# Performance work log

Hardware: AMD Instinct MI355X
Metric: run time of the kernel (lower is better)

The kernel has to match this reference:

```python
import jax, jax.numpy as jnp
import numpy as np

K_MASK = -2.3819763e+38
B, T, D = 2, 2048, 2048
N, K, H = 8, 2, 256          # query heads, kv heads, head dim
F = 8192                     # ffn hidden
A = 4                        # num_altup_inputs
P = 4                        # num_modalities
WINDOW = 512
SOFT_CAP = 50.0
Q_SCALE = H ** -0.5
ROPE_BASE = 10000.0


def rms_norm(x, scale=None, eps=1e-6):
    y = x * jax.lax.rsqrt(jnp.mean(jnp.square(x), axis=-1, keepdims=True) + eps)
    if scale is not None:
        y = y * (1.0 + scale)   # scale_plus_one=True
    return y


def apply_rope(x, pos, base=ROPE_BASE, scale_factor=1.0):
    # x: [B,T,num_heads,H], pos: [B,T]
    h = x.shape[-1]
    frac = 2.0 * jnp.arange(h // 2, dtype=jnp.float32) / h
    timescale = base ** frac
    sin_inp = (pos[..., None].astype(jnp.float32) / timescale)[..., None, :] / scale_factor  # [B,T,1,H/2]
    sin, cos = jnp.sin(sin_inp), jnp.cos(sin_inp)
    x1, x2 = jnp.split(x, 2, axis=-1)
    return jnp.concatenate([x1 * cos - x2 * sin, x2 * cos + x1 * sin], axis=-1).astype(x.dtype)


def setup_inputs():
    key = jax.random.key(0)
    ks = jax.random.split(key, 12)
    r = lambda i, shape, s=0.02: jax.random.normal(ks[i], shape, dtype=jnp.float32) * s
    pos = jnp.broadcast_to(jnp.arange(T, dtype=jnp.int32), (B, T))
    causal = pos[:, :, None] >= pos[:, None, :]  # [B,T,T] bool
    return dict(
        x=jax.random.normal(ks[0], (A, B, T, D), dtype=jnp.float32),
        segment_pos=pos,
        attn_mask=causal,
        router_w=r(1, (D, P), 1.0),
        pred_coefs=r(2, (P, A, A), 0.0001),
        corr_coefs=r(3, (P, A), 0.01),
        correct_output_scale=jnp.ones((D,), jnp.float32),
        pre_attn_scale=jnp.zeros((D,), jnp.float32),
        q_w=r(4, (N, D, H)),
        kv_w=r(5, (2, K, D, H)),
        qk_q_scale=jnp.zeros((H,), jnp.float32),
        qk_k_scale=jnp.zeros((H,), jnp.float32),
        o_w=r(6, (N, H, D)),
        post_attn_scale=jnp.zeros((D,), jnp.float32),
        pre_ffw_scale=jnp.zeros((D,), jnp.float32),
        gate_w=r(7, (D, F)),
        up_w=r(8, (D, F)),
        down_w=r(9, (F, D)),
        post_ffw_scale=jnp.zeros((D,), jnp.float32),
    )


def _router(h, router_w):
    # modality router: scale by 1/d_model, project, tanh in fp32
    return jnp.tanh(jnp.einsum('btd,dp->btp', h * (1.0 / D), router_w).astype(jnp.float32))


def _attention(x, segment_pos, attn_mask, q_w, kv_w, qk_q_scale, qk_k_scale, o_w):
    q = jnp.einsum('btd,ndh->btnh', x, q_w)               # [B,T,N,H]
    k, v = jnp.einsum('bsd,ckdh->cbskh', x, kv_w)         # each [B,T,K,H]
    q = rms_norm(q, qk_q_scale)                           # qk norm
    k = rms_norm(k, qk_k_scale)
    v = rms_norm(v)                                       # value norm (no scale)
    q = apply_rope(q, segment_pos) * Q_SCALE
    k = apply_rope(k, segment_pos)
    g = N // K                                            # GQA group size
    qr = q.reshape(B, T, K, g, H)
    logits = jnp.einsum('btkgh,bskh->btkgs', qr, k).reshape(B, T, N, T)
    logits = jnp.tanh(logits / SOFT_CAP) * SOFT_CAP       # attn_logits_soft_cap
    # sliding-window mask combined with causal attn_mask
    sliding = (segment_pos[:, None, :] > segment_pos[:, :, None] - WINDOW) & \
              (segment_pos[:, None, :] < segment_pos[:, :, None] + WINDOW)
    mask = attn_mask & sliding
    padded = jnp.where(mask[:, :, None, :], logits, K_MASK)
    probs = jax.nn.softmax(padded, axis=-1).astype(k.dtype)
    enc = jnp.einsum('btkgs,bskh->btkgh', probs.reshape(B, T, K, g, T), v).reshape(B, T, N, H)
    return jnp.einsum('btnh,nhd->btd', enc, o_w)


def reference(x, segment_pos, attn_mask, router_w, pred_coefs, corr_coefs,
              correct_output_scale, pre_attn_scale, q_w, kv_w, qk_q_scale, qk_k_scale,
              o_w, post_attn_scale, pre_ffw_scale, gate_w, up_w, down_w, post_ffw_scale):
    # ---- AltUp predict ----
    mods = _router(x[0], router_w)                                   # [B,T,P]
    coefs = jnp.einsum('btp,pij->btij', mods, pred_coefs.astype(jnp.float32))
    predictions = x + jnp.einsum('btij,jbtd->ibtd', coefs, x).astype(x.dtype)
    active = predictions[0]
    # ---- attention block ----
    attn_in = rms_norm(active, pre_attn_scale)
    attn = _attention(attn_in, segment_pos, attn_mask, q_w, kv_w, qk_q_scale, qk_k_scale, o_w)
    attn = rms_norm(attn, post_attn_scale)
    attn_gated = active + attn
    # ---- gated-GELU MLP ----
    h = rms_norm(attn_gated, pre_ffw_scale)
    ffw = jnp.einsum('btf,fd->btd', jax.nn.gelu(h @ gate_w) * (h @ up_w), down_w)
    ffw = rms_norm(ffw, post_ffw_scale)
    activated = attn_gated + ffw
    # ---- AltUp correct (with scale_corrected_output) ----
    activated = activated * correct_output_scale
    mods_c = _router(activated, router_w)
    c = jnp.einsum('btp,pi->bti', mods_c, corr_coefs.astype(jnp.float32)) + 1.0
    innovation = activated - predictions[0]
    corrected = predictions + jnp.einsum('bti,btd->ibtd', c, innovation).astype(x.dtype)
    return corrected
```

## Files before the change

### kernel.cpp

```cpp
#include <hip/hip_runtime.h>
#include <hip/hip_bf16.h>

typedef unsigned short u16;
typedef __attribute__((ext_vector_type(8))) short bf16x8_t;
typedef __attribute__((ext_vector_type(4))) float f32x4_t;

#define DEV __device__ __forceinline__

constexpr int cB = 2, cT = 2048, cD = 2048;
constexpr int cN = 8, cK = 2, cH = 256, cF = 8192;
constexpr int cBT = cB * cT;
constexpr float cEPS = 1e-6f;
constexpr float cQS = 0.0625f;
constexpr float cCAP = 50.0f;
constexpr int cWIN = 512;
constexpr int cNH = 12;

DEV u16 f2bf(float f) {
  union { float f; unsigned u; } c; c.f = f;
  unsigned u = c.u;
  return (u16)((u + 0x7fffu + ((u >> 16) & 1u)) >> 16);
}
DEV float bf2f(u16 h) {
  union { unsigned u; float f; } c; c.u = ((unsigned)h) << 16;
  return c.f;
}

DEV float block_sum256(float v, float* sbuf) {
  #pragma unroll
  for (int m = 32; m > 0; m >>= 1) v += __shfl_xor(v, m, 64);
  int wid = threadIdx.x >> 6;
  if ((threadIdx.x & 63) == 0) sbuf[wid] = v;
  __syncthreads();
  float tot = sbuf[0] + sbuf[1] + sbuf[2] + sbuf[3];
  __syncthreads();
  return tot;
}

#define GLD_LDS16(gp, lp) __builtin_amdgcn_global_load_lds( \
    (const __attribute__((address_space(1))) void*)(gp),    \
    (__attribute__((address_space(3))) void*)(lp), 16, 0, 0)

#define WAITV(n) asm volatile("s_waitcnt vmcnt(" #n ")" ::: "memory")
#define LGKM0()  asm volatile("s_waitcnt lgkmcnt(0)" ::: "memory")

__global__ __launch_bounds__(256) void k_transpose_cast(
    const float* __restrict__ src, u16* __restrict__ dst, int R, int C) {
  __shared__ float tile[32][33];
  size_t base = (size_t)blockIdx.z * R * C;
  int c0 = blockIdx.x * 32, r0 = blockIdx.y * 32;
  int tx = threadIdx.x & 31, ty = threadIdx.x >> 5;
  #pragma unroll
  for (int i = 0; i < 4; i++)
    tile[ty + i * 8][tx] = src[base + (size_t)(r0 + ty + i * 8) * C + c0 + tx];
  __syncthreads();
  #pragma unroll
  for (int i = 0; i < 4; i++)
    dst[base + (size_t)(c0 + ty + i * 8) * R + r0 + tx] = f2bf(tile[tx][ty + i * 8]);
}

__global__ __launch_bounds__(256) void k_predict(
    const float* __restrict__ x, const float* __restrict__ router_w,
    const float* __restrict__ pred_coefs, const float* __restrict__ pre_attn_scale,
    float* __restrict__ out, u16* __restrict__ attn_in) {
  __shared__ float sbuf[4];
  int bt = blockIdx.x, tid = threadIdx.x;
  const size_t PL = (size_t)cBT * cD;
  const size_t rowb = (size_t)bt * cD;
  float xv[4][8];
  #pragma unroll
  for (int j = 0; j < 4; j++)
    #pragma unroll
    for (int u = 0; u < 8; u++)
      xv[j][u] = x[j * PL + rowb + u * 256 + tid];
  float rp0 = 0, rp1 = 0, rp2 = 0, rp3 = 0;
  #pragma unroll
  for (int u = 0; u < 8; u++) {
    const float4 rw = *(const float4*)(router_w + (size_t)(u * 256 + tid) * 4);
    rp0 += xv[0][u] * rw.x; rp1 += xv[0][u] * rw.y;
    rp2 += xv[0][u] * rw.z; rp3 += xv[0][u] * rw.w;
  }
  float mods[4];
  mods[0] = tanhf(block_sum256(rp0, sbuf) * (1.0f / cD));
  mods[1] = tanhf(block_sum256(rp1, sbuf) * (1.0f / cD));
  mods[2] = tanhf(block_sum256(rp2, sbuf) * (1.0f / cD));
  mods[3] = tanhf(block_sum256(rp3, sbuf) * (1.0f / cD));
  float coef[4][4];
  #pragma unroll
  for (int i = 0; i < 4; i++)
    #pragma unroll
    for (int j = 0; j < 4; j++) {
      float s = 0;
      #pragma unroll
      for (int p = 0; p < 4; p++) s += mods[p] * pred_coefs[(p * 4 + i) * 4 + j];
      coef[i][j] = s;
    }
  float p0[8], ssq = 0;
  #pragma unroll
  for (int u = 0; u < 8; u++) {
    #pragma unroll
    for (int i = 0; i < 4; i++) {
      float s = xv[i][u];
      #pragma unroll
      for (int j = 0; j < 4; j++) s += coef[i][j] * xv[j][u];
      out[i * PL + rowb + u * 256 + tid] = s;
      if (i == 0) { p0[u] = s; ssq += s * s; }
    }
  }
  float rs = rsqrtf(block_sum256(ssq, sbuf) * (1.0f / cD) + cEPS);
  #pragma unroll
  for (int u = 0; u < 8; u++) {
    int d = u * 256 + tid;
    attn_in[rowb + d] = f2bf(p0[u] * rs * (1.0f + pre_attn_scale[d]));
  }
}

template <int MI, int OUT_BF16>
__global__ __launch_bounds__(512, 2) void k_gemm8(
    const u16* __restrict__ A, const u16* __restrict__ Bt, void* __restrict__ Cv,
    int Nn, int Kk) {
  static_assert(MI == 4 || MI == 8, "");
  constexpr int BM = MI * 32;
  constexpr int A_KS = BM * 32;
  constexpr int B_KS = 256 * 32;
  constexpr int BUF_E = 2 * A_KS + 2 * B_KS;
  extern __shared__ u16 lds[];

  const int tid = threadIdx.x;
  const int wid = tid >> 6, lane = tid & 63;
  const int wr = wid >> 2, wc = wid & 3;
  const int fr = lane & 15, fq = lane >> 4;

  const int nwg = gridDim.x * gridDim.y;
  const int flat = blockIdx.y * gridDim.x + blockIdx.x;
  const int swz = (flat & 7) * (nwg >> 3) + (flat >> 3);
  const int m0 = (swz % gridDim.x) * BM;
  const int n0 = (swz / gridDim.x) * 256;
  const int NT = Kk >> 6;

  const int srow = lane >> 2, sslot = lane & 3;

  auto stageA = [&](int t, int ks) {
    u16* buf = lds + (t & 1) * BUF_E + ks * A_KS;
    #pragma unroll
    for (int i = 0; i < BM / 128; i++) {
      int row0 = i * 128 + wid * 16;
      int row = row0 + srow;
      int col = (sslot ^ ((row >> 1) & 3)) * 8;
      GLD_LDS16(A + (size_t)(m0 + row) * Kk + t * 64 + ks * 32 + col, buf + row0 * 32);
    }
  };
  auto stageB = [&](int t, int ks) {
    u16* buf = lds + (t & 1) * BUF_E + 2 * A_KS + ks * B_KS;
    #pragma unroll
    for (int i = 0; i < 2; i++) {
      int row0 = i * 128 + wid * 16;
      int row = row0 + srow;
      int col = (sslot ^ ((row >> 1) & 3)) * 8;
      GLD_LDS16(Bt + (size_t)(n0 + row) * Kk + t * 64 + ks * 32 + col, buf + row0 * 32);
    }
  };
  auto readA = [&](const u16* buf, int ks, int i) -> bf16x8_t {
    int row = wr * (MI * 16) + i * 16 + fr;
    return *(const bf16x8_t*)(buf + ks * A_KS + row * 32 + (fq ^ ((row >> 1) & 3)) * 8);
  };
  auto readB = [&](const u16* buf, int ks, int j) -> bf16x8_t {
    int row = wc * 64 + j * 16 + fr;
    return *(const bf16x8_t*)(buf + 2 * A_KS + ks * B_KS + row * 32 + (fq ^ ((row >> 1) & 3)) * 8);
  };

  f32x4_t acc[MI][4];
  #pragma unroll
  for (int i = 0; i < MI; i++)
    #pragma unroll
    for (int j = 0; j < 4; j++) acc[i][j] = (f32x4_t){0.f, 0.f, 0.f, 0.f};

  stageA(0, 0); stageB(0, 0); stageA(0, 1); stageB(0, 1);
  if constexpr (MI == 8) WAITV(4); else WAITV(3);
  __builtin_amdgcn_s_barrier();

#define PHASE_MFMA(J0)                                                              \
  __builtin_amdgcn_s_setprio(1);                                                    \
  _Pragma("unroll")                                                                 \
  for (int i = 0; i < MI; i++) {                                                    \
    acc[i][J0]     = __builtin_amdgcn_mfma_f32_16x16x32_bf16(a0[i], b0[0], acc[i][J0], 0, 0, 0);     \
    acc[i][J0 + 1] = __builtin_amdgcn_mfma_f32_16x16x32_bf16(a0[i], b0[1], acc[i][J0 + 1], 0, 0, 0); \
  }                                                                                 \
  __builtin_amdgcn_s_setprio(0);

  for (int t = 0; t < NT; t++) {
    const u16* buf = lds + (t & 1) * BUF_E;
    const bool pf = (t + 1 < NT);
    bf16x8_t a0[MI], b0[2];

    #pragma unroll
    for (int i = 0; i < MI; i++) a0[i] = readA(buf, 0, i);
    b0[0] = readB(buf, 0, 0); b0[1] = readB(buf, 0, 1);
    if (pf) stageA(t + 1, 0);
    __builtin_amdgcn_s_barrier();
    LGKM0(); __builtin_amdgcn_sched_barrier(0);
    PHASE_MFMA(0)
    __builtin_amdgcn_s_barrier();

    b0[0] = readB(buf, 0, 2); b0[1] = readB(buf, 0, 3);
    if (pf) stageB(t + 1, 0);
    if (pf) { if constexpr (MI == 8) WAITV(4); else WAITV(3); } else WAITV(0);
    __builtin_amdgcn_s_barrier();
    LGKM0(); __builtin_amdgcn_sched_barrier(0);
    PHASE_MFMA(2)
    __builtin_amdgcn_s_barrier();

    #pragma unroll
    for (int i = 0; i < MI; i++) a0[i] = readA(buf, 1, i);
    b0[0] = readB(buf, 1, 0); b0[1] = readB(buf, 1, 1);
    if (pf) stageA(t + 1, 1);
    __builtin_amdgcn_s_barrier();
    LGKM0(); __builtin_amdgcn_sched_barrier(0);
    PHASE_MFMA(0)
    __builtin_amdgcn_s_barrier();

    b0[0] = readB(buf, 1, 2); b0[1] = readB(buf, 1, 3);
    if (pf) stageB(t + 1, 1);
    if (pf) { if constexpr (MI == 8) WAITV(4); else WAITV(3); }
    __builtin_amdgcn_s_barrier();
    LGKM0(); __builtin_amdgcn_sched_barrier(0);
    PHASE_MFMA(2)
    __builtin_amdgcn_s_barrier();
  }
#undef PHASE_MFMA

  #pragma unroll
  for (int i = 0; i < MI; i++)
    #pragma unroll
    for (int j = 0; j < 4; j++)
      #pragma unroll
      for (int r = 0; r < 4; r++) {
        int m = m0 + wr * (MI * 16) + i * 16 + fq * 4 + r;
        int n = n0 + wc * 64 + j * 16 + fr;
        float v = acc[i][j][r];
        if (OUT_BF16) ((u16*)Cv)[(size_t)m * Nn + n] = f2bf(v);
        else ((float*)Cv)[(size_t)m * Nn + n] = v;
      }
}

__global__ __launch_bounds__(64) void k_qkpost(
    u16* __restrict__ buf, const float* __restrict__ scale, const int* __restrict__ pos,
    int heads, int tokstride, int headoff, float oscale) {
  int hidx = blockIdx.x % heads, bt = blockIdx.x / heads;
  int lane = threadIdx.x;
  u16* row = buf + ((size_t)bt * tokstride + headoff + hidx) * cH;
  float v[4], ssq = 0;
  #pragma unroll
  for (int m = 0; m < 4; m++) { v[m] = bf2f(row[lane + 64 * m]); ssq += v[m] * v[m]; }
  #pragma unroll
  for (int mm = 32; mm > 0; mm >>= 1) ssq += __shfl_xor(ssq, mm, 64);
  float rs = rsqrtf(ssq * (1.0f / cH) + cEPS);
  #pragma unroll
  for (int m = 0; m < 4; m++) {
    int e = lane + 64 * m;
    v[m] = v[m] * rs * (1.0f + scale[e]);
  }
  float p = (float)pos[bt];
  #pragma unroll
  for (int m = 0; m < 2; m++) {
    int j = lane + 64 * m;
    float ts = powf(10000.0f, (2.0f * j) * (1.0f / cH));
    float si = p / ts;
    float sn = sinf(si), cs = cosf(si);
    float x1 = v[m], x2 = v[m + 2];
    row[j]       = f2bf((x1 * cs - x2 * sn) * oscale);
    row[j + 128] = f2bf((x2 * cs + x1 * sn) * oscale);
  }
}

__global__ __launch_bounds__(64) void k_vpost(
    const u16* __restrict__ qkv, u16* __restrict__ vT) {
  int kk = blockIdx.x % cK, bt = blockIdx.x / cK;
  int b = bt / cT, t = bt % cT;
  int lane = threadIdx.x;
  const u16* row = qkv + ((size_t)bt * cNH + 10 + kk) * cH;
  float v[4], ssq = 0;
  #pragma unroll
  for (int m = 0; m < 4; m++) { v[m] = bf2f(row[lane + 64 * m]); ssq += v[m] * v[m]; }
  #pragma unroll
  for (int mm = 32; mm > 0; mm >>= 1) ssq += __shfl_xor(ssq, mm, 64);
  float rs = rsqrtf(ssq * (1.0f / cH) + cEPS);
  #pragma unroll
  for (int m = 0; m < 4; m++) {
    int e = lane + 64 * m;
    vT[((size_t)(b * cK + kk) * cH + e) * cT + t] = f2bf(v[m] * rs);
  }
}

__global__ __launch_bounds__(64) void k_attn(
    const u16* __restrict__ qkv, const u16* __restrict__ vT, u16* __restrict__ enc) {
  int t0 = blockIdx.x * 16;
  int n = blockIdx.y, b = blockIdx.z;
  int kn = n >> 2;
  int lane = threadIdx.x;
  int fr = lane & 15, fq = lane >> 4;
  __shared__ float P[16][32];

  bf16x8_t qf[8];
  const u16* qrow = qkv + ((size_t)(b * cT + t0 + fr) * cNH + n) * cH;
  #pragma unroll
  for (int ks = 0; ks < 8; ks++) qf[ks] = *(const bf16x8_t*)(qrow + ks * 32 + fq * 8);

  f32x4_t acc[16];
  #pragma unroll
  for (int ht = 0; ht < 16; ht++) acc[ht] = (f32x4_t){0.f, 0.f, 0.f, 0.f};
  float psum[4] = {0.f, 0.f, 0.f, 0.f};

  int s_lo = t0 - (cWIN - 1); if (s_lo < 0) s_lo = 0; s_lo &= ~31;
  for (int s0 = s_lo; s0 <= t0 + 15; s0 += 32) {
    f32x4_t S[2];
    S[0] = (f32x4_t){0.f, 0.f, 0.f, 0.f};
    S[1] = (f32x4_t){0.f, 0.f, 0.f, 0.f};
    #pragma unroll
    for (int c = 0; c < 2; c++) {
      const u16* krow = qkv + ((size_t)(b * cT + s0 + c * 16 + fr) * cNH + 8 + kn) * cH;
      #pragma unroll
      for (int ks = 0; ks < 8; ks++) {
        bf16x8_t kf = *(const bf16x8_t*)(krow + ks * 32 + fq * 8);
        S[c] = __builtin_amdgcn_mfma_f32_16x16x32_bf16(qf[ks], kf, S[c], 0, 0, 0);
      }
    }
    #pragma unroll
    for (int c = 0; c < 2; c++) {
      int s = s0 + c * 16 + fr;
      #pragma unroll
      for (int r = 0; r < 4; r++) {
        int t = t0 + fq * 4 + r;
        float l = S[c][r];
        l = tanhf(l * (1.0f / cCAP)) * cCAP;
        float pe = (s <= t && s >= t - (cWIN - 1)) ? __expf(l) : 0.0f;
        psum[r] += pe;
        P[fq * 4 + r][c * 16 + fr] = pe;
      }
    }
    bf16x8_t pf;
    #pragma unroll
    for (int e = 0; e < 8; e++) pf[e] = (short)f2bf(P[fr][fq * 8 + e]);
    #pragma unroll
    for (int ht = 0; ht < 16; ht++) {
      bf16x8_t vf = *(const bf16x8_t*)(vT + (((size_t)(b * cK + kn)) * cH + ht * 16 + fr) * cT + s0 + fq * 8);
      acc[ht] = __builtin_amdgcn_mfma_f32_16x16x32_bf16(pf, vf, acc[ht], 0, 0, 0);
    }
  }
  #pragma unroll
  for (int r = 0; r < 4; r++) {
    #pragma unroll
    for (int m = 1; m < 16; m <<= 1) psum[r] += __shfl_xor(psum[r], m, 64);
  }
  float inv[4];
  #pragma unroll
  for (int r = 0; r < 4; r++) inv[r] = 1.0f / psum[r];
  #pragma unroll
  for (int ht = 0; ht < 16; ht++)
    #pragma unroll
    for (int r = 0; r < 4; r++)
      enc[(((size_t)(b * cT + t0 + fq * 4 + r)) * cN + n) * cH + ht * 16 + fr] =
          f2bf(acc[ht][r] * inv[r]);
}

__global__ __launch_bounds__(256) void k_postattn(
    const float* __restrict__ attn_raw, const float* __restrict__ out0,
    const float* __restrict__ post_attn_scale, const float* __restrict__ pre_ffw_scale,
    float* __restrict__ ag, u16* __restrict__ h) {
  __shared__ float sbuf[4];
  int bt = blockIdx.x, tid = threadIdx.x;
  const size_t rowb = (size_t)bt * cD;
  float ar[8], ssq = 0;
  #pragma unroll
  for (int u = 0; u < 8; u++) { ar[u] = attn_raw[rowb + u * 256 + tid]; ssq += ar[u] * ar[u]; }
  float rs = rsqrtf(block_sum256(ssq, sbuf) * (1.0f / cD) + cEPS);
  float agv[8], ssq2 = 0;
  #pragma unroll
  for (int u = 0; u < 8; u++) {
    int d = u * 256 + tid;
    float a = out0[rowb + d] + ar[u] * rs * (1.0f + post_attn_scale[d]);
    agv[u] = a;
    ag[rowb + d] = a;
    ssq2 += a * a;
  }
  float rs2 = rsqrtf(block_sum256(ssq2, sbuf) * (1.0f / cD) + cEPS);
  #pragma unroll
  for (int u = 0; u < 8; u++) {
    int d = u * 256 + tid;
    h[rowb + d] = f2bf(agv[u] * rs2 * (1.0f + pre_ffw_scale[d]));
  }
}

__global__ __launch_bounds__(256) void k_gelumul(
    const u16* __restrict__ GU, u16* __restrict__ Ap) {
  size_t i = (size_t)blockIdx.x * 256 + threadIdx.x;
  size_t row = i >> 10, col8 = i & 1023;
  const u16* gp = GU + row * (2 * cF) + col8 * 8;
  bf16x8_t g8 = *(const bf16x8_t*)gp;
  bf16x8_t u8 = *(const bf16x8_t*)(gp + cF);
  bf16x8_t o;
  #pragma unroll
  for (int e = 0; e < 8; e++) {
    float xg = bf2f((u16)g8[e]);
    float xu = bf2f((u16)u8[e]);
    float t = 0.5f * xg * (1.0f + tanhf(0.7978845608f * (xg + 0.044715f * xg * xg * xg)));
    o[e] = (short)f2bf(t * xu);
  }
  *(bf16x8_t*)(Ap + row * cF + col8 * 8) = o;
}

__global__ __launch_bounds__(256) void k_final(
    const float* __restrict__ ffw_raw, const float* __restrict__ ag,
    const float* __restrict__ post_ffw_scale, const float* __restrict__ cos_scale,
    const float* __restrict__ router_w, const float* __restrict__ corr_coefs,
    float* __restrict__ out) {
  __shared__ float sbuf[4];
  int bt = blockIdx.x, tid = threadIdx.x;
  const size_t PL = (size_t)cBT * cD;
  const size_t rowb = (size_t)bt * cD;
  float fv[8], ssq = 0;
  #pragma unroll
  for (int u = 0; u < 8; u++) { fv[u] = ffw_raw[rowb + u * 256 + tid]; ssq += fv[u] * fv[u]; }
  float rs = rsqrtf(block_sum256(ssq, sbuf) * (1.0f / cD) + cEPS);
  float av[8];
  float rp0 = 0, rp1 = 0, rp2 = 0, rp3 = 0;
  #pragma unroll
  for (int u = 0; u < 8; u++) {
    int d = u * 256 + tid;
    float a = (ag[rowb + d] + fv[u] * rs * (1.0f + post_ffw_scale[d])) * cos_scale[d];
    av[u] = a;
    const float4 rw = *(const float4*)(router_w + (size_t)d * 4);
    rp0 += a * rw.x; rp1 += a * rw.y; rp2 += a * rw.z; rp3 += a * rw.w;
  }
  float mods[4];
  mods[0] = tanhf(block_sum256(rp0, sbuf) * (1.0f / cD));
  mods[1] = tanhf(block_sum256(rp1, sbuf) * (1.0f / cD));
  mods[2] = tanhf(block_sum256(rp2, sbuf) * (1.0f / cD));
  mods[3] = tanhf(block_sum256(rp3, sbuf) * (1.0f / cD));
  float cc[4];
  #pragma unroll
  for (int i = 0; i < 4; i++) {
    float s = 1.0f;
    #pragma unroll
    for (int p = 0; p < 4; p++) s += mods[p] * corr_coefs[p * 4 + i];
    cc[i] = s;
  }
  #pragma unroll
  for (int u = 0; u < 8; u++) {
    size_t o = rowb + u * 256 + tid;
    float p0v = out[o];
    float innov = av[u] - p0v;
    out[o] = p0v + cc[0] * innov;
    out[PL + o]     += cc[1] * innov;
    out[2 * PL + o] += cc[2] * innov;
    out[3 * PL + o] += cc[3] * innov;
  }
}

extern "C" void kernel_launch(void* const* d_in, const int* in_sizes, int n_in,
                              void* d_out, int out_size, void* d_ws, size_t ws_size,
                              hipStream_t stream) {
  const float* x              = (const float*)d_in[0];
  const int*   pos            = (const int*)d_in[1];
  const float* router_w       = (const float*)d_in[3];
  const float* pred_coefs     = (const float*)d_in[4];
  const float* corr_coefs     = (const float*)d_in[5];
  const float* cos_scale      = (const float*)d_in[6];
  const float* pre_attn_scale = (const float*)d_in[7];
  const float* q_w            = (const float*)d_in[8];
  const float* kv_w           = (const float*)d_in[9];
  const float* qk_q_scale     = (const float*)d_in[10];
  const float* qk_k_scale     = (const float*)d_in[11];
  const float* o_w            = (const float*)d_in[12];
  const float* post_attn_scale= (const float*)d_in[13];
  const float* pre_ffw_scale  = (const float*)d_in[14];
  const float* gate_w         = (const float*)d_in[15];
  const float* up_w           = (const float*)d_in[16];
  const float* down_w         = (const float*)d_in[17];
  const float* post_ffw_scale = (const float*)d_in[18];
  float* out = (float*)d_out;

  char* wsp = (char*)d_ws;
  size_t off = 0;
  auto take = [&](size_t nbytes) -> char* {
    char* p = wsp + off;
    off += (nbytes + 255) & ~((size_t)255);
    return p;
  };
  u16* gu_wT    = (u16*)take((size_t)2 * cF * cD * 2);
  u16* down_wT  = (u16*)take((size_t)cD * cF * 2);
  u16* qkv_wT   = (u16*)take((size_t)cNH * cH * cD * 2);
  u16* o_wT     = (u16*)take((size_t)cD * cN * cH * 2);
  u16* attn_in  = (u16*)take((size_t)cBT * cD * 2);
  u16* qkvbuf   = (u16*)take((size_t)cBT * cNH * cH * 2);
  u16* vTbuf    = (u16*)take((size_t)cB * cK * cH * cT * 2);
  u16* encbuf   = (u16*)take((size_t)cBT * cN * cH * 2);
  float* attn_raw = (float*)take((size_t)cBT * cD * 4);
  float* agbuf    = (float*)take((size_t)cBT * cD * 4);
  u16* hbuf     = (u16*)take((size_t)cBT * cD * 2);
  u16* GUbuf    = (u16*)take((size_t)cBT * 2 * cF * 2);
  u16* Gcbuf    = (u16*)take((size_t)cBT * cF * 2);
  float* ffw_raw = (float*)take((size_t)cBT * cD * 4);
  (void)in_sizes; (void)n_in; (void)out_size; (void)ws_size;

  dim3 blk256(256), blk64(64), blk512(512);
  constexpr unsigned LDS8 = 2 * (2 * 256 * 32 + 2 * 256 * 32) * 2;
  constexpr unsigned LDS4 = 2 * (2 * 128 * 32 + 2 * 256 * 32) * 2;

  k_transpose_cast<<<dim3(cF / 32, cD / 32, 1), blk256, 0, stream>>>(gate_w, gu_wT, cD, cF);
  k_transpose_cast<<<dim3(cF / 32, cD / 32, 1), blk256, 0, stream>>>(up_w, gu_wT + (size_t)cF * cD, cD, cF);
  k_transpose_cast<<<dim3(cD / 32, cF / 32, 1), blk256, 0, stream>>>(down_w, down_wT, cF, cD);
  k_transpose_cast<<<dim3(cH / 32, cD / 32, cN), blk256, 0, stream>>>(q_w, qkv_wT, cD, cH);
  k_transpose_cast<<<dim3(cH / 32, cD / 32, 2 * cK), blk256, 0, stream>>>(
      kv_w, qkv_wT + (size_t)cN * cH * cD, cD, cH);
  k_transpose_cast<<<dim3(cD / 32, (cN * cH) / 32, 1), blk256, 0, stream>>>(o_w, o_wT, cN * cH, cD);

  k_predict<<<dim3(cBT), blk256, 0, stream>>>(x, router_w, pred_coefs, pre_attn_scale, out, attn_in);

  k_gemm8<4, 1><<<dim3(cBT / 128, (cNH * cH) / 256), blk512, LDS4, stream>>>(
      attn_in, qkv_wT, qkvbuf, cNH * cH, cD);

  k_qkpost<<<dim3(cBT * cN), blk64, 0, stream>>>(qkvbuf, qk_q_scale, pos, cN, cNH, 0, cQS);
  k_qkpost<<<dim3(cBT * cK), blk64, 0, stream>>>(qkvbuf, qk_k_scale, pos, cK, cNH, 8, 1.0f);
  k_vpost<<<dim3(cBT * cK), blk64, 0, stream>>>(qkvbuf, vTbuf);

  k_attn<<<dim3(cT / 16, cN, cB), blk64, 0, stream>>>(qkvbuf, vTbuf, encbuf);

  k_gemm8<4, 0><<<dim3(cBT / 128, cD / 256), blk512, LDS4, stream>>>(
      encbuf, o_wT, attn_raw, cD, cN * cH);
  k_postattn<<<dim3(cBT), blk256, 0, stream>>>(attn_raw, out, post_attn_scale, pre_ffw_scale, agbuf, hbuf);

  k_gemm8<8, 1><<<dim3(cBT / 256, (2 * cF) / 256), blk512, LDS8, stream>>>(
      hbuf, gu_wT, GUbuf, 2 * cF, cD);
  k_gelumul<<<dim3((unsigned)(((size_t)cBT * cF / 8) / 256)), blk256, 0, stream>>>(GUbuf, Gcbuf);
  k_gemm8<4, 0><<<dim3(cBT / 128, cD / 256), blk512, LDS4, stream>>>(
      Gcbuf, down_wT, ffw_raw, cD, cF);

  k_final<<<dim3(cBT), blk256, 0, stream>>>(ffw_raw, agbuf, post_ffw_scale, cos_scale,
                                            router_w, corr_coefs, out);
}
```

Baseline: 1.046 ms.

## Fuse GELU-gate multiply into gate/up GEMM epilogue via interleaved weights; vectorize row kernels

```diff
diff --git a/kernel.cpp b/kernel.cpp
--- a/kernel.cpp
+++ b/kernel.cpp
@@ -25,6 +25,15 @@
   union { unsigned u; float f; } c; c.u = ((unsigned)h) << 16;
   return c.f;
 }
+DEV float g4(const float4& v, int k) { return k == 0 ? v.x : k == 1 ? v.y : k == 2 ? v.z : v.w; }
+DEV void store_bf4(u16* p, float a, float b, float c, float d) {
+  union { u16 h[4]; uint2 v; } o;
+  o.h[0] = f2bf(a); o.h[1] = f2bf(b); o.h[2] = f2bf(c); o.h[3] = f2bf(d);
+  *(uint2*)p = o.v;
+}
+DEV float gelu_tanh(float x) {
+  return 0.5f * x * (1.0f + tanhf(0.7978845608f * (x + 0.044715f * x * x * x)));
+}
 
 DEV float block_sum256(float v, float* sbuf) {
   #pragma unroll
@@ -45,7 +54,7 @@
 #define LGKM0()  asm volatile("s_waitcnt lgkmcnt(0)" ::: "memory")
 
 __global__ __launch_bounds__(256) void k_transpose_cast(
-    const float* __restrict__ src, u16* __restrict__ dst, int R, int C) {
+    const float* __restrict__ src, u16* __restrict__ dst, int R, int C, int gu) {
   __shared__ float tile[32][33];
   size_t base = (size_t)blockIdx.z * R * C;
   int c0 = blockIdx.x * 32, r0 = blockIdx.y * 32;
@@ -55,8 +64,11 @@
     tile[ty + i * 8][tx] = src[base + (size_t)(r0 + ty + i * 8) * C + c0 + tx];
   __syncthreads();
   #pragma unroll
-  for (int i = 0; i < 4; i++)
-    dst[base + (size_t)(c0 + ty + i * 8) * R + r0 + tx] = f2bf(tile[tx][ty + i * 8]);
+  for (int i = 0; i < 4; i++) {
+    int c = c0 + ty + i * 8;
+    int n = (gu < 0) ? c : (((c >> 4) << 5) + (gu << 4) + (c & 15));
+    dst[base + (size_t)n * R + r0 + tx] = f2bf(tile[tx][ty + i * 8]);
+  }
 }
 
 __global__ __launch_bounds__(256) void k_predict(
@@ -67,24 +79,25 @@
   int bt = blockIdx.x, tid = threadIdx.x;
   const size_t PL = (size_t)cBT * cD;
   const size_t rowb = (size_t)bt * cD;
-  float xv[4][8];
+  float4 xv[4][2];
   #pragma unroll
   for (int j = 0; j < 4; j++)
     #pragma unroll
-    for (int u = 0; u < 8; u++)
-      xv[j][u] = x[j * PL + rowb + u * 256 + tid];
-  float rp0 = 0, rp1 = 0, rp2 = 0, rp3 = 0;
-  #pragma unroll
-  for (int u = 0; u < 8; u++) {
-    const float4 rw = *(const float4*)(router_w + (size_t)(u * 256 + tid) * 4);
-    rp0 += xv[0][u] * rw.x; rp1 += xv[0][u] * rw.y;
-    rp2 += xv[0][u] * rw.z; rp3 += xv[0][u] * rw.w;
-  }
+    for (int u = 0; u < 2; u++)
+      xv[j][u] = *(const float4*)(x + j * PL + rowb + (u * 256 + tid) * 4);
+  float rp[4] = {0, 0, 0, 0};
+  #pragma unroll
+  for (int u = 0; u < 2; u++)
+    #pragma unroll
+    for (int k = 0; k < 4; k++) {
+      int e = (u * 256 + tid) * 4 + k;
+      float4 rw = *(const float4*)(router_w + (size_t)e * 4);
+      float xe = g4(xv[0][u], k);
+      rp[0] += xe * rw.x; rp[1] += xe * rw.y; rp[2] += xe * rw.z; rp[3] += xe * rw.w;
+    }
   float mods[4];
-  mods[0] = tanhf(block_sum256(rp0, sbuf) * (1.0f / cD));
-  mods[1] = tanhf(block_sum256(rp1, sbuf) * (1.0f / cD));
-  mods[2] = tanhf(block_sum256(rp2, sbuf) * (1.0f / cD));
-  mods[3] = tanhf(block_sum256(rp3, sbuf) * (1.0f / cD));
+  #pragma unroll
+  for (int p = 0; p < 4; p++) mods[p] = tanhf(block_sum256(rp[p], sbuf) * (1.0f / cD));
   float coef[4][4];
   #pragma unroll
   for (int i = 0; i < 4; i++)
@@ -95,27 +108,32 @@
       for (int p = 0; p < 4; p++) s += mods[p] * pred_coefs[(p * 4 + i) * 4 + j];
       coef[i][j] = s;
     }
-  float p0[8], ssq = 0;
-  #pragma unroll
-  for (int u = 0; u < 8; u++) {
+  float4 p04[2]; float ssq = 0;
+  #pragma unroll
+  for (int u = 0; u < 2; u++)
     #pragma unroll
     for (int i = 0; i < 4; i++) {
-      float s = xv[i][u];
+      float4 s = xv[i][u];
       #pragma unroll
-      for (int j = 0; j < 4; j++) s += coef[i][j] * xv[j][u];
-      out[i * PL + rowb + u * 256 + tid] = s;
-      if (i == 0) { p0[u] = s; ssq += s * s; }
-    }
-  }
+      for (int j = 0; j < 4; j++) {
+        s.x += coef[i][j] * xv[j][u].x; s.y += coef[i][j] * xv[j][u].y;
+        s.z += coef[i][j] * xv[j][u].z; s.w += coef[i][j] * xv[j][u].w;
+      }
+      *(float4*)(out + i * PL + rowb + (u * 256 + tid) * 4) = s;
+      if (i == 0) { p04[u] = s; ssq += s.x * s.x + s.y * s.y + s.z * s.z + s.w * s.w; }
+    }
   float rs = rsqrtf(block_sum256(ssq, sbuf) * (1.0f / cD) + cEPS);
   #pragma unroll
-  for (int u = 0; u < 8; u++) {
-    int d = u * 256 + tid;
-    attn_in[rowb + d] = f2bf(p0[u] * rs * (1.0f + pre_attn_scale[d]));
-  }
-}
-
-template <int MI, int OUT_BF16>
+  for (int u = 0; u < 2; u++) {
+    int e0 = (u * 256 + tid) * 4;
+    float4 sc = *(const float4*)(pre_attn_scale + e0);
+    store_bf4(attn_in + rowb + e0,
+              p04[u].x * rs * (1.0f + sc.x), p04[u].y * rs * (1.0f + sc.y),
+              p04[u].z * rs * (1.0f + sc.z), p04[u].w * rs * (1.0f + sc.w));
+  }
+}
+
+template <int MI, int OUT_MODE>
 __global__ __launch_bounds__(512, 2) void k_gemm8(
     const u16* __restrict__ A, const u16* __restrict__ Bt, void* __restrict__ Cv,
     int Nn, int Kk) {
@@ -229,18 +247,34 @@
   }
 #undef PHASE_MFMA
 
-  #pragma unroll
-  for (int i = 0; i < MI; i++)
-    #pragma unroll
-    for (int j = 0; j < 4; j++)
+  if constexpr (OUT_MODE == 2) {
+    const int Nh = Nn >> 1;
+    #pragma unroll
+    for (int i = 0; i < MI; i++)
       #pragma unroll
-      for (int r = 0; r < 4; r++) {
-        int m = m0 + wr * (MI * 16) + i * 16 + fq * 4 + r;
-        int n = n0 + wc * 64 + j * 16 + fr;
-        float v = acc[i][j][r];
-        if (OUT_BF16) ((u16*)Cv)[(size_t)m * Nn + n] = f2bf(v);
-        else ((float*)Cv)[(size_t)m * Nn + n] = v;
+      for (int jp = 0; jp < 2; jp++) {
+        int c = (n0 + wc * 64 + jp * 32) / 2 + fr;
+        #pragma unroll
+        for (int r = 0; r < 4; r++) {
+          int m = m0 + wr * (MI * 16) + i * 16 + fq * 4 + r;
+          float g = acc[i][2 * jp][r], uu = acc[i][2 * jp + 1][r];
+          ((u16*)Cv)[(size_t)m * Nh + c] = f2bf(gelu_tanh(g) * uu);
+        }
       }
+  } else {
+    #pragma unroll
+    for (int i = 0; i < MI; i++)
+      #pragma unroll
+      for (int j = 0; j < 4; j++)
+        #pragma unroll
+        for (int r = 0; r < 4; r++) {
+          int m = m0 + wr * (MI * 16) + i * 16 + fq * 4 + r;
+          int n = n0 + wc * 64 + j * 16 + fr;
+          float v = acc[i][j][r];
+          if (OUT_MODE == 1) ((u16*)Cv)[(size_t)m * Nn + n] = f2bf(v);
+          else ((float*)Cv)[(size_t)m * Nn + n] = v;
+        }
+  }
 }
 
 __global__ __launch_bounds__(64) void k_qkpost(
@@ -370,43 +404,37 @@
   __shared__ float sbuf[4];
   int bt = blockIdx.x, tid = threadIdx.x;
   const size_t rowb = (size_t)bt * cD;
-  float ar[8], ssq = 0;
-  #pragma unroll
-  for (int u = 0; u < 8; u++) { ar[u] = attn_raw[rowb + u * 256 + tid]; ssq += ar[u] * ar[u]; }
+  float4 ar[2]; float ssq = 0;
+  #pragma unroll
+  for (int u = 0; u < 2; u++) {
+    ar[u] = *(const float4*)(attn_raw + rowb + (u * 256 + tid) * 4);
+    ssq += ar[u].x * ar[u].x + ar[u].y * ar[u].y + ar[u].z * ar[u].z + ar[u].w * ar[u].w;
+  }
   float rs = rsqrtf(block_sum256(ssq, sbuf) * (1.0f / cD) + cEPS);
-  float agv[8], ssq2 = 0;
-  #pragma unroll
-  for (int u = 0; u < 8; u++) {
-    int d = u * 256 + tid;
-    float a = out0[rowb + d] + ar[u] * rs * (1.0f + post_attn_scale[d]);
+  float4 agv[2]; float ssq2 = 0;
+  #pragma unroll
+  for (int u = 0; u < 2; u++) {
+    int e0 = (u * 256 + tid) * 4;
+    float4 o0 = *(const float4*)(out0 + rowb + e0);
+    float4 sc = *(const float4*)(post_attn_scale + e0);
+    float4 a;
+    a.x = o0.x + ar[u].x * rs * (1.0f + sc.x);
+    a.y = o0.y + ar[u].y * rs * (1.0f + sc.y);
+    a.z = o0.z + ar[u].z * rs * (1.0f + sc.z);
+    a.w = o0.w + ar[u].w * rs * (1.0f + sc.w);
     agv[u] = a;
-    ag[rowb + d] = a;
-    ssq2 += a * a;
+    *(float4*)(ag + rowb + e0) = a;
+    ssq2 += a.x * a.x + a.y * a.y + a.z * a.z + a.w * a.w;
   }
   float rs2 = rsqrtf(block_sum256(ssq2, sbuf) * (1.0f / cD) + cEPS);
   #pragma unroll
-  for (int u = 0; u < 8; u++) {
-    int d = u * 256 + tid;
-    h[rowb + d] = f2bf(agv[u] * rs2 * (1.0f + pre_ffw_scale[d]));
-  }
-}
-
-__global__ __launch_bounds__(256) void k_gelumul(
-    const u16* __restrict__ GU, u16* __restrict__ Ap) {
-  size_t i = (size_t)blockIdx.x * 256 + threadIdx.x;
-  size_t row = i >> 10, col8 = i & 1023;
-  const u16* gp = GU + row * (2 * cF) + col8 * 8;
-  bf16x8_t g8 = *(const bf16x8_t*)gp;
-  bf16x8_t u8 = *(const bf16x8_t*)(gp + cF);
-  bf16x8_t o;
-  #pragma unroll
-  for (int e = 0; e < 8; e++) {
-    float xg = bf2f((u16)g8[e]);
-    float xu = bf2f((u16)u8[e]);
-    float t = 0.5f * xg * (1.0f + tanhf(0.7978845608f * (xg + 0.044715f * xg * xg * xg)));
-    o[e] = (short)f2bf(t * xu);
-  }
-  *(bf16x8_t*)(Ap + row * cF + col8 * 8) = o;
+  for (int u = 0; u < 2; u++) {
+    int e0 = (u * 256 + tid) * 4;
+    float4 sc = *(const float4*)(pre_ffw_scale + e0);
+    store_bf4(h + rowb + e0,
+              agv[u].x * rs2 * (1.0f + sc.x), agv[u].y * rs2 * (1.0f + sc.y),
+              agv[u].z * rs2 * (1.0f + sc.z), agv[u].w * rs2 * (1.0f + sc.w));
+  }
 }
 
 __global__ __launch_bounds__(256) void k_final(
@@ -418,25 +446,37 @@
   int bt = blockIdx.x, tid = threadIdx.x;
   const size_t PL = (size_t)cBT * cD;
   const size_t rowb = (size_t)bt * cD;
-  float fv[8], ssq = 0;
-  #pragma unroll
-  for (int u = 0; u < 8; u++) { fv[u] = ffw_raw[rowb + u * 256 + tid]; ssq += fv[u] * fv[u]; }
+  float4 fv[2]; float ssq = 0;
+  #pragma unroll
+  for (int u = 0; u < 2; u++) {
+    fv[u] = *(const float4*)(ffw_raw + rowb + (u * 256 + tid) * 4);
+    ssq += fv[u].x * fv[u].x + fv[u].y * fv[u].y + fv[u].z * fv[u].z + fv[u].w * fv[u].w;
+  }
   float rs = rsqrtf(block_sum256(ssq, sbuf) * (1.0f / cD) + cEPS);
-  float av[8];
-  float rp0 = 0, rp1 = 0, rp2 = 0, rp3 = 0;
-  #pragma unroll
-  for (int u = 0; u < 8; u++) {
-    int d = u * 256 + tid;
-    float a = (ag[rowb + d] + fv[u] * rs * (1.0f + post_ffw_scale[d])) * cos_scale[d];
+  float4 av[2];
+  float rp[4] = {0, 0, 0, 0};
+  #pragma unroll
+  for (int u = 0; u < 2; u++) {
+    int e0 = (u * 256 + tid) * 4;
+    float4 agx = *(const float4*)(ag + rowb + e0);
+    float4 ps = *(const float4*)(post_ffw_scale + e0);
+    float4 cs = *(const float4*)(cos_scale + e0);
+    float4 a;
+    a.x = (agx.x + fv[u].x * rs * (1.0f + ps.x)) * cs.x;
+    a.y = (agx.y + fv[u].y * rs * (1.0f + ps.y)) * cs.y;
+    a.z = (agx.z + fv[u].z * rs * (1.0f + ps.z)) * cs.z;
+    a.w = (agx.w + fv[u].w * rs * (1.0f + ps.w)) * cs.w;
     av[u] = a;
-    const float4 rw = *(const float4*)(router_w + (size_t)d * 4);
-    rp0 += a * rw.x; rp1 += a * rw.y; rp2 += a * rw.z; rp3 += a * rw.w;
+    #pragma unroll
+    for (int k = 0; k < 4; k++) {
+      float4 rw = *(const float4*)(router_w + (size_t)(e0 + k) * 4);
+      float xe = g4(a, k);
+      rp[0] += xe * rw.x; rp[1] += xe * rw.y; rp[2] += xe * rw.z; rp[3] += xe * rw.w;
+    }
   }
   float mods[4];
-  mods[0] = tanhf(block_sum256(rp0, sbuf) * (1.0f / cD));
-  mods[1] = tanhf(block_sum256(rp1, sbuf) * (1.0f / cD));
-  mods[2] = tanhf(block_sum256(rp2, sbuf) * (1.0f / cD));
-  mods[3] = tanhf(block_sum256(rp3, sbuf) * (1.0f / cD));
+  #pragma unroll
+  for (int p = 0; p < 4; p++) mods[p] = tanhf(block_sum256(rp[p], sbuf) * (1.0f / cD));
   float cc[4];
   #pragma unroll
   for (int i = 0; i < 4; i++) {
@@ -446,14 +486,23 @@
     cc[i] = s;
   }
   #pragma unroll
-  for (int u = 0; u < 8; u++) {
-    size_t o = rowb + u * 256 + tid;
-    float p0v = out[o];
-    float innov = av[u] - p0v;
-    out[o] = p0v + cc[0] * innov;
-    out[PL + o]     += cc[1] * innov;
-    out[2 * PL + o] += cc[2] * innov;
-    out[3 * PL + o] += cc[3] * innov;
+  for (int u = 0; u < 2; u++) {
+    size_t o = rowb + (u * 256 + tid) * 4;
+    float4 p0 = *(const float4*)(out + o);
+    float4 in4;
+    in4.x = av[u].x - p0.x; in4.y = av[u].y - p0.y;
+    in4.z = av[u].z - p0.z; in4.w = av[u].w - p0.w;
+    float4 w0;
+    w0.x = p0.x + cc[0] * in4.x; w0.y = p0.y + cc[0] * in4.y;
+    w0.z = p0.z + cc[0] * in4.z; w0.w = p0.w + cc[0] * in4.w;
+    *(float4*)(out + o) = w0;
+    #pragma unroll
+    for (int i = 1; i < 4; i++) {
+      float4 q = *(const float4*)(out + i * PL + o);
+      q.x += cc[i] * in4.x; q.y += cc[i] * in4.y;
+      q.z += cc[i] * in4.z; q.w += cc[i] * in4.w;
+      *(float4*)(out + i * PL + o) = q;
+    }
   }
 }
 
@@ -498,7 +547,6 @@
   float* attn_raw = (float*)take((size_t)cBT * cD * 4);
   float* agbuf    = (float*)take((size_t)cBT * cD * 4);
   u16* hbuf     = (u16*)take((size_t)cBT * cD * 2);
-  u16* GUbuf    = (u16*)take((size_t)cBT * 2 * cF * 2);
   u16* Gcbuf    = (u16*)take((size_t)cBT * cF * 2);
   float* ffw_raw = (float*)take((size_t)cBT * cD * 4);
   (void)in_sizes; (void)n_in; (void)out_size; (void)ws_size;
@@ -507,13 +555,13 @@
   constexpr unsigned LDS8 = 2 * (2 * 256 * 32 + 2 * 256 * 32) * 2;
   constexpr unsigned LDS4 = 2 * (2 * 128 * 32 + 2 * 256 * 32) * 2;
 
-  k_transpose_cast<<<dim3(cF / 32, cD / 32, 1), blk256, 0, stream>>>(gate_w, gu_wT, cD, cF);
-  k_transpose_cast<<<dim3(cF / 32, cD / 32, 1), blk256, 0, stream>>>(up_w, gu_wT + (size_t)cF * cD, cD, cF);
-  k_transpose_cast<<<dim3(cD / 32, cF / 32, 1), blk256, 0, stream>>>(down_w, down_wT, cF, cD);
-  k_transpose_cast<<<dim3(cH / 32, cD / 32, cN), blk256, 0, stream>>>(q_w, qkv_wT, cD, cH);
+  k_transpose_cast<<<dim3(cF / 32, cD / 32, 1), blk256, 0, stream>>>(gate_w, gu_wT, cD, cF, 0);
+  k_transpose_cast<<<dim3(cF / 32, cD / 32, 1), blk256, 0, stream>>>(up_w, gu_wT, cD, cF, 1);
+  k_transpose_cast<<<dim3(cD / 32, cF / 32, 1), blk256, 0, stream>>>(down_w, down_wT, cF, cD, -1);
+  k_transpose_cast<<<dim3(cH / 32, cD / 32, cN), blk256, 0, stream>>>(q_w, qkv_wT, cD, cH, -1);
   k_transpose_cast<<<dim3(cH / 32, cD / 32, 2 * cK), blk256, 0, stream>>>(
-      kv_w, qkv_wT + (size_t)cN * cH * cD, cD, cH);
-  k_transpose_cast<<<dim3(cD / 32, (cN * cH) / 32, 1), blk256, 0, stream>>>(o_w, o_wT, cN * cH, cD);
+      kv_w, qkv_wT + (size_t)cN * cH * cD, cD, cH, -1);
+  k_transpose_cast<<<dim3(cD / 32, (cN * cH) / 32, 1), blk256, 0, stream>>>(o_w, o_wT, cN * cH, cD, -1);
 
   k_predict<<<dim3(cBT), blk256, 0, stream>>>(x, router_w, pred_coefs, pre_attn_scale, out, attn_in);
 
@@ -530,9 +578,8 @@
       encbuf, o_wT, attn_raw, cD, cN * cH);
   k_postattn<<<dim3(cBT), blk256, 0, stream>>>(attn_raw, out, post_attn_scale, pre_ffw_scale, agbuf, hbuf);
 
-  k_gemm8<8, 1><<<dim3(cBT / 256, (2 * cF) / 256), blk512, LDS8, stream>>>(
-      hbuf, gu_wT, GUbuf, 2 * cF, cD);
-  k_gelumul<<<dim3((unsigned)(((size_t)cBT * cF / 8) / 256)), blk256, 0, stream>>>(GUbuf, Gcbuf);
+  k_gemm8<8, 2><<<dim3(cBT / 256, (2 * cF) / 256), blk512, LDS8, stream>>>(
+      hbuf, gu_wT, Gcbuf, 2 * cF, cD);
   k_gemm8<4, 0><<<dim3(cBT / 128, cD / 256), blk512, LDS4, stream>>>(
       Gcbuf, down_wT, ffw_raw, cD, cF);
 
```

Result: faster. 1.000 ms (-4.3%).
